# Performance work log

Hardware: AMD Instinct MI355X
Metric: run time of the kernel (lower is better)

The kernel has to match this reference:

```python
import jax, jax.numpy as jnp
import numpy as np

FEATURE_SIZE = 1000000  # padding index == FEATURE_SIZE
NEG_INF = -1e9


def _attn_pool(emb_table, hist_idx, ad_idx):
    # hist_idx: [B, L] int, ad_idx: [B] int
    hist = emb_table[hist_idx]          # [B, L, K] gather
    ad = emb_table[ad_idx]              # [B, K]
    score = jnp.einsum('blk,bk->bl', hist, ad)          # [B, L]
    score = jnp.where(hist_idx != FEATURE_SIZE, score, NEG_INF)
    w = jax.nn.softmax(score, axis=1)
    return jnp.einsum('blk,bl->bk', hist, w)            # [B, K]


def setup_inputs() -> dict:
    key = jax.random.key(0)
    ks = jax.random.split(key, 12)
    B, F, K = 4096, 8, 64
    V = FEATURE_SIZE + 1
    d_in = 3 * K + F * K  # 704
    inp = {
        'feature_idx': jax.random.randint(ks[0], (B, F), 0, FEATURE_SIZE),
        'hist_item': jax.random.randint(ks[1], (B, 350), 0, V),
        'hist_author': jax.random.randint(ks[2], (B, 250), 0, V),
        'hist_music': jax.random.randint(ks[3], (B, 100), 0, V),
        'emb_table': jax.random.normal(ks[4], (V, K), jnp.float32),
        'W1': jax.random.normal(ks[5], (d_in, 512), jnp.float32) * 0.02,
        'b1': jnp.zeros((512,), jnp.float32),
        'W2': jax.random.normal(ks[6], (512, 256), jnp.float32) * 0.02,
        'b2': jnp.zeros((256,), jnp.float32),
        'W3': jax.random.normal(ks[7], (256, 128), jnp.float32) * 0.02,
        'b3': jnp.zeros((128,), jnp.float32),
        'Wo': jax.random.normal(ks[8], (128, 1), jnp.float32) * 0.02,
        'bo': jnp.zeros((1,), jnp.float32),
    }
    return inp


def reference(feature_idx, hist_item, hist_author, hist_music, emb_table,
              W1, b1, W2, b2, W3, b3, Wo, bo):
    # ad indices for the three behavior features: columns 2, 3, 6
    pools = [
        _attn_pool(emb_table, hist_item, feature_idx[:, 2]),
        _attn_pool(emb_table, hist_author, feature_idx[:, 3]),
        _attn_pool(emb_table, hist_music, feature_idx[:, 6]),
    ]
    user_beha = jnp.concatenate(pools, axis=1)                    # [B, 3K]
    B = feature_idx.shape[0]
    ad_emb = emb_table[feature_idx].reshape(B, -1)                # [B, F*K]
    x = jnp.concatenate([user_beha, ad_emb], axis=1)              # [B, 704]
    x = jax.nn.relu(x @ W1 + b1)
    x = jax.nn.relu(x @ W2 + b2)
    x = jax.nn.relu(x @ W3 + b3)
    logits = x @ Wo + bo                                          # [B, 1]
    return logits
```

## Files before the change

kernel.cpp:

```cpp
#include <hip/hip_runtime.h>
#include <cstddef>

#define BATCH   4096
#define PAD_IDX 1000000
#define NEG_INF_F (-1e9f)

typedef __attribute__((ext_vector_type(8))) short bf16x8;
typedef __attribute__((ext_vector_type(4))) float f32x4;
typedef unsigned short u16;

__device__ __forceinline__ u16 f2bf(float f) {
    unsigned u = __float_as_uint(f);
    return (u16)((u + 0x7fffu + ((u >> 16) & 1u)) >> 16);
}
__device__ __forceinline__ float bf2f(u16 b) {
    return __uint_as_float(((unsigned)b) << 16);
}

#define UPD(mm, dd, aa, s, v)                          \
    {                                                  \
        float nm = fmaxf(mm, (s));                     \
        float sc = __expf(mm - nm);                    \
        float e  = __expf((s) - nm);                   \
        dd = fmaf(dd, sc, e);                          \
        aa.x = fmaf(aa.x, sc, e * (v).x);              \
        aa.y = fmaf(aa.y, sc, e * (v).y);              \
        aa.z = fmaf(aa.z, sc, e * (v).z);              \
        aa.w = fmaf(aa.w, sc, e * (v).w);              \
        mm = nm;                                       \
    }

#define MERGE(P)                                                  \
    {                                                             \
        float mo  = __shfl_xor(m, P);                             \
        float d_o = __shfl_xor(d, P);                             \
        float ax = __shfl_xor(acc.x, P);                          \
        float ay = __shfl_xor(acc.y, P);                          \
        float az = __shfl_xor(acc.z, P);                          \
        float aw = __shfl_xor(acc.w, P);                          \
        float nm = fmaxf(m, mo);                                  \
        float sA = __expf(m - nm), sB = __expf(mo - nm);          \
        d = d * sA + d_o * sB;                                    \
        acc.x = acc.x * sA + ax * sB;                             \
        acc.y = acc.y * sA + ay * sB;                             \
        acc.z = acc.z * sA + az * sB;                             \
        acc.w = acc.w * sA + aw * sB;                             \
        m = nm;                                                   \
    }

#define QRED(s)                       \
    s += __shfl_xor(s, 1);            \
    s += __shfl_xor(s, 2);            \
    s += __shfl_xor(s, 4);            \
    s += __shfl_xor(s, 8);

#define DOT4(v, a) ((v).x * (a).x + (v).y * (a).y + (v).z * (a).z + (v).w * (a).w)

__global__ void __launch_bounds__(256) prep_kernel(
    const int* __restrict__ fidx,
    const int* __restrict__ hist_item,
    const int* __restrict__ hist_author,
    const int* __restrict__ hist_music,
    const float* __restrict__ emb,
    const float* __restrict__ W1, const float* __restrict__ W2, const float* __restrict__ W3,
    u16* __restrict__ x,
    u16* __restrict__ w1t, u16* __restrict__ w2t, u16* __restrict__ w3t)
{
    __shared__ float tile[32][33];
    const int blk = blockIdx.x;

    if (blk < 5120) {
        const int w    = blk * 4 + (threadIdx.x >> 6);
        const int lane = threadIdx.x & 63;
        const int t16  = lane & 15;
        const int q    = lane >> 4;

        if (w < 3 * BATCH) {
            const int h = w >> 12;
            const int b = w & (BATCH - 1);
            int L, col, off;
            const int* hrow;
            if (h == 0)      { L = 350; col = 2; off = 0;   hrow = hist_item   + (size_t)b * 350; }
            else if (h == 1) { L = 250; col = 3; off = 64;  hrow = hist_author + (size_t)b * 250; }
            else             { L = 100; col = 6; off = 128; hrow = hist_music  + (size_t)b * 100; }

            const int ad_idx = fidx[b * 8 + col];
            const float4 ad4 = *(const float4*)(emb + (size_t)ad_idx * 64 + 4 * t16);

            float m = NEG_INF_F, d = 0.f;
            float4 acc = make_float4(0.f, 0.f, 0.f, 0.f);
            float mB = NEG_INF_F, dB = 0.f;
            float4 aB = make_float4(0.f, 0.f, 0.f, 0.f);

            int l = 0;
            if (L >= 16) {
                int n0 = hrow[q], n1 = hrow[4 + q], n2 = hrow[8 + q], n3 = hrow[12 + q];
                while (true) {
                    const int i0 = n0, i1 = n1, i2 = n2, i3 = n3;
                    const float4 v0 = *(const float4*)(emb + (size_t)i0 * 64 + 4 * t16);
                    const float4 v1 = *(const float4*)(emb + (size_t)i1 * 64 + 4 * t16);
                    const float4 v2 = *(const float4*)(emb + (size_t)i2 * 64 + 4 * t16);
                    const float4 v3 = *(const float4*)(emb + (size_t)i3 * 64 + 4 * t16);
                    l += 16;
                    const bool more = (l + 16 <= L);
                    if (more) {
                        n0 = hrow[l + q];      n1 = hrow[l + 4 + q];
                        n2 = hrow[l + 8 + q];  n3 = hrow[l + 12 + q];
                    }
                    float s0 = DOT4(v0, ad4);
                    float s1 = DOT4(v1, ad4);
                    float s2 = DOT4(v2, ad4);
                    float s3 = DOT4(v3, ad4);
                    QRED(s0) QRED(s1) QRED(s2) QRED(s3)
                    if (i0 == PAD_IDX) s0 = NEG_INF_F;
                    if (i1 == PAD_IDX) s1 = NEG_INF_F;
                    if (i2 == PAD_IDX) s2 = NEG_INF_F;
                    if (i3 == PAD_IDX) s3 = NEG_INF_F;
                    UPD(m, d, acc, s0, v0)
                    UPD(mB, dB, aB, s1, v1)
                    UPD(m, d, acc, s2, v2)
                    UPD(mB, dB, aB, s3, v3)
                    if (!more) break;
                }
            }
            for (; l < L; l += 4) {
                const int li = l + q;
                const int i0 = (li < L) ? hrow[li] : PAD_IDX;
                const float4 v0 = *(const float4*)(emb + (size_t)i0 * 64 + 4 * t16);
                float s0 = DOT4(v0, ad4);
                QRED(s0)
                if (i0 == PAD_IDX) s0 = NEG_INF_F;
                UPD(m, d, acc, s0, v0)
            }

            {
                float nm = fmaxf(m, mB);
                float eA = __expf(m - nm), eB = __expf(mB - nm);
                d = d * eA + dB * eB;
                acc.x = acc.x * eA + aB.x * eB;
                acc.y = acc.y * eA + aB.y * eB;
                acc.z = acc.z * eA + aB.z * eB;
                acc.w = acc.w * eA + aB.w * eB;
                m = nm;
            }
            MERGE(16)
            MERGE(32)

            if (lane < 16) {
                const float inv = 1.f / d;
                uint2 p;
                p.x = (unsigned)f2bf(acc.x * inv) | ((unsigned)f2bf(acc.y * inv) << 16);
                p.y = (unsigned)f2bf(acc.z * inv) | ((unsigned)f2bf(acc.w * inv) << 16);
                *(uint2*)(x + (size_t)b * 704 + off + 4 * t16) = p;
            }
        } else {
            const int tt = w - 3 * BATCH;
            const int b  = tt >> 1;
            const int f  = ((tt & 1) << 2) + q;
            const int idx = fidx[b * 8 + f];
            const float4 v = *(const float4*)(emb + (size_t)idx * 64 + 4 * t16);
            uint2 p;
            p.x = (unsigned)f2bf(v.x) | ((unsigned)f2bf(v.y) << 16);
            p.y = (unsigned)f2bf(v.z) | ((unsigned)f2bf(v.w) << 16);
            *(uint2*)(x + (size_t)b * 704 + 192 + (size_t)f * 64 + 4 * t16) = p;
        }
    } else {
        int t = blk - 5120;
        const float* W; u16* WT; int K, N, tk, tn;
        if (t < 352)      { W = W1; WT = w1t; K = 704; N = 512; tk = t % 22; tn = t / 22; }
        else if (t < 480) { t -= 352; W = W2; WT = w2t; K = 512; N = 256; tk = t % 16; tn = t / 16; }
        else              { t -= 480; W = W3; WT = w3t; K = 256; N = 128; tk = t % 8;  tn = t / 8;  }
        const int k0 = tk * 32, n0 = tn * 32;
        const int tx = threadIdx.x & 31, ty = threadIdx.x >> 5;
#pragma unroll
        for (int j = 0; j < 4; ++j)
            tile[ty + 8 * j][tx] = W[(size_t)(k0 + ty + 8 * j) * N + n0 + tx];
        __syncthreads();
#pragma unroll
        for (int j = 0; j < 4; ++j)
            WT[(size_t)(n0 + ty + 8 * j) * K + k0 + tx] = f2bf(tile[tx][ty + 8 * j]);
    }
}

template <int BN>
__global__ void __launch_bounds__(256) gemm_mfma(
    const u16* __restrict__ A, const u16* __restrict__ BT,
    const float* __restrict__ bias, u16* __restrict__ C,
    int M, int N, int K)
{
    constexpr int NB = BN / 16;
    __shared__ u16 As[64][40];
    __shared__ u16 Bs[BN][40];

    const int tid  = threadIdx.x;
    const int wave = tid >> 6, lane = tid & 63;
    const int quad = lane >> 4, l16 = lane & 15;
    const int bm = blockIdx.y * 64, bn = blockIdx.x * BN;

    const int srow = tid >> 2;
    const int sk   = (tid & 3) * 8;

    f32x4 acc[NB];
#pragma unroll
    for (int i = 0; i < NB; ++i) acc[i] = (f32x4){0.f, 0.f, 0.f, 0.f};

    const size_t a_base = (size_t)(bm + srow) * K + sk;

    for (int k0 = 0; k0 < K; k0 += 32) {
        *(float4*)&As[srow][sk] = *(const float4*)(A + a_base + k0);
#pragma unroll
        for (int r0 = 0; r0 < BN; r0 += 64) {
            *(float4*)&Bs[r0 + srow][sk] =
                *(const float4*)(BT + (size_t)(bn + r0 + srow) * K + k0 + sk);
        }
        __syncthreads();

        const bf16x8 af = *(const bf16x8*)&As[wave * 16 + l16][quad * 8];
#pragma unroll
        for (int ni = 0; ni < NB; ++ni) {
            const bf16x8 bf = *(const bf16x8*)&Bs[ni * 16 + l16][quad * 8];
            acc[ni] = __builtin_amdgcn_mfma_f32_16x16x32_bf16(af, bf, acc[ni], 0, 0, 0);
        }
        __syncthreads();
    }

#pragma unroll
    for (int ni = 0; ni < NB; ++ni) {
        const int col = bn + ni * 16 + l16;
        const float bv = bias[col];
#pragma unroll
        for (int r = 0; r < 4; ++r) {
            const int row = bm + wave * 16 + quad * 4 + r;
            float v = fmaxf(acc[ni][r] + bv, 0.f);
            C[(size_t)row * N + col] = f2bf(v);
        }
    }
}

__global__ void __launch_bounds__(256) gemm3_out(
    const u16* __restrict__ A, const u16* __restrict__ BT,
    const float* __restrict__ bias,
    const float* __restrict__ Wo, const float* __restrict__ bo,
    float* __restrict__ out)
{
    constexpr int K = 256, NB = 8;
    __shared__ u16 As[64][40];
    __shared__ u16 Bs[128][40];

    const int tid  = threadIdx.x;
    const int wave = tid >> 6, lane = tid & 63;
    const int quad = lane >> 4, l16 = lane & 15;
    const int bm = blockIdx.x * 64;

    const int srow = tid >> 2;
    const int sk   = (tid & 3) * 8;

    f32x4 acc[NB];
#pragma unroll
    for (int i = 0; i < NB; ++i) acc[i] = (f32x4){0.f, 0.f, 0.f, 0.f};

    const size_t a_base = (size_t)(bm + srow) * K + sk;

    for (int k0 = 0; k0 < K; k0 += 32) {
        *(float4*)&As[srow][sk] = *(const float4*)(A + a_base + k0);
#pragma unroll
        for (int r0 = 0; r0 < 128; r0 += 64) {
            *(float4*)&Bs[r0 + srow][sk] =
                *(const float4*)(BT + (size_t)(r0 + srow) * K + k0 + sk);
        }
        __syncthreads();

        const bf16x8 af = *(const bf16x8*)&As[wave * 16 + l16][quad * 8];
#pragma unroll
        for (int ni = 0; ni < NB; ++ni) {
            const bf16x8 bf = *(const bf16x8*)&Bs[ni * 16 + l16][quad * 8];
            acc[ni] = __builtin_amdgcn_mfma_f32_16x16x32_bf16(af, bf, acc[ni], 0, 0, 0);
        }
        __syncthreads();
    }

    float part[4] = {0.f, 0.f, 0.f, 0.f};
#pragma unroll
    for (int ni = 0; ni < NB; ++ni) {
        const int col = ni * 16 + l16;
        const float bv = bias[col];
        const float wv = Wo[col];
#pragma unroll
        for (int r = 0; r < 4; ++r)
            part[r] = fmaf(fmaxf(acc[ni][r] + bv, 0.f), wv, part[r]);
    }
#pragma unroll
    for (int r = 0; r < 4; ++r) {
        part[r] += __shfl_xor(part[r], 1);
        part[r] += __shfl_xor(part[r], 2);
        part[r] += __shfl_xor(part[r], 4);
        part[r] += __shfl_xor(part[r], 8);
    }
    if (l16 == 0) {
        const float b0 = bo[0];
#pragma unroll
        for (int r = 0; r < 4; ++r)
            out[bm + wave * 16 + quad * 4 + r] = part[r] + b0;
    }
}

extern "C" void kernel_launch(void* const* d_in, const int* in_sizes, int n_in,
                              void* d_out, int out_size, void* d_ws, size_t ws_size,
                              hipStream_t stream) {
    const int*   fidx  = (const int*)d_in[0];
    const int*   hitem = (const int*)d_in[1];
    const int*   hauth = (const int*)d_in[2];
    const int*   hmus  = (const int*)d_in[3];
    const float* emb   = (const float*)d_in[4];
    const float* W1 = (const float*)d_in[5];
    const float* b1 = (const float*)d_in[6];
    const float* W2 = (const float*)d_in[7];
    const float* b2 = (const float*)d_in[8];
    const float* W3 = (const float*)d_in[9];
    const float* b3 = (const float*)d_in[10];
    const float* Wo = (const float*)d_in[11];
    const float* bo = (const float*)d_in[12];
    float* out = (float*)d_out;

    u16* x   = (u16*)d_ws;
    u16* h1  = x   + (size_t)BATCH * 704;
    u16* h2  = h1  + (size_t)BATCH * 512;
    u16* w1t = h2  + (size_t)BATCH * 256;
    u16* w2t = w1t + (size_t)704 * 512;
    u16* w3t = w2t + (size_t)512 * 256;

    prep_kernel<<<5632, 256, 0, stream>>>(fidx, hitem, hauth, hmus, emb,
                                          W1, W2, W3, x, w1t, w2t, w3t);

    gemm_mfma<64><<<dim3(512 / 64, BATCH / 64), 256, 0, stream>>>(
        x, w1t, b1, h1, BATCH, 512, 704);
    gemm_mfma<64><<<dim3(256 / 64, BATCH / 64), 256, 0, stream>>>(
        h1, w2t, b2, h2, BATCH, 256, 512);
    gemm3_out<<<BATCH / 64, 256, 0, stream>>>(h2, w3t, b3, Wo, bo, out);
}
```

Baseline: 445.3 us.

## Prefetch embedding table into cache and fuse the layer-2/3/output GEMMs

Adds 2048 leading blocks to the prep kernel that stream-read the whole embedding table, so that the random row gathers of the attention pooling are more likely to hit the large last-level cache. A dummy conditional store keeps the compiler from removing these reads. Separately, the second and third MLP layers and the output projection are merged into one tail kernel over 16-row tiles that keeps h2 in shared memory, which removes a launch and the h2 round trip through global memory. The cost is an extra full-table read of about 256 MB, and each tail block re-reading all of W2T/W3T with smaller tiles.

```diff
diff --git a/kernel.cpp b/kernel.cpp
--- a/kernel.cpp
+++ b/kernel.cpp
@@ -4,6 +4,7 @@
 #define BATCH   4096
 #define PAD_IDX 1000000
 #define NEG_INF_F (-1e9f)
+#define EMB_FLOATS 64000064
 
 typedef __attribute__((ext_vector_type(8))) short bf16x8;
 typedef __attribute__((ext_vector_type(4))) float f32x4;
@@ -12,9 +13,6 @@
 __device__ __forceinline__ u16 f2bf(float f) {
     unsigned u = __float_as_uint(f);
     return (u16)((u + 0x7fffu + ((u >> 16) & 1u)) >> 16);
-}
-__device__ __forceinline__ float bf2f(u16 b) {
-    return __uint_as_float(((unsigned)b) << 16);
 }
 
 #define UPD(mm, dd, aa, s, v)                          \
@@ -68,10 +66,26 @@
 {
     __shared__ float tile[32][33];
     const int blk = blockIdx.x;
-
-    if (blk < 5120) {
-        const int w    = blk * 4 + (threadIdx.x >> 6);
-        const int lane = threadIdx.x & 63;
+    const int tid = threadIdx.x;
+
+    if (blk < 2048) {
+        float s = 0.f;
+        const size_t base = (size_t)blk * 32768 + tid * 4;
+#pragma unroll 8
+        for (int i = 0; i < 32; ++i) {
+            const size_t fi = base + (size_t)i * 1024;
+            if (fi + 4 <= EMB_FLOATS) {
+                const float4 v = *(const float4*)(emb + fi);
+                s += v.x + v.y + v.z + v.w;
+            }
+        }
+        if (s == 1.2345e37f) x[0] = 1;
+        return;
+    }
+
+    if (blk < 7168) {
+        const int w    = (blk - 2048) * 4 + (tid >> 6);
+        const int lane = tid & 63;
         const int t16  = lane & 15;
         const int q    = lane >> 4;
 
@@ -164,22 +178,23 @@
             p.y = (unsigned)f2bf(v.z) | ((unsigned)f2bf(v.w) << 16);
             *(uint2*)(x + (size_t)b * 704 + 192 + (size_t)f * 64 + 4 * t16) = p;
         }
-    } else {
-        int t = blk - 5120;
-        const float* W; u16* WT; int K, N, tk, tn;
-        if (t < 352)      { W = W1; WT = w1t; K = 704; N = 512; tk = t % 22; tn = t / 22; }
-        else if (t < 480) { t -= 352; W = W2; WT = w2t; K = 512; N = 256; tk = t % 16; tn = t / 16; }
-        else              { t -= 480; W = W3; WT = w3t; K = 256; N = 128; tk = t % 8;  tn = t / 8;  }
-        const int k0 = tk * 32, n0 = tn * 32;
-        const int tx = threadIdx.x & 31, ty = threadIdx.x >> 5;
-#pragma unroll
-        for (int j = 0; j < 4; ++j)
-            tile[ty + 8 * j][tx] = W[(size_t)(k0 + ty + 8 * j) * N + n0 + tx];
-        __syncthreads();
-#pragma unroll
-        for (int j = 0; j < 4; ++j)
-            WT[(size_t)(n0 + ty + 8 * j) * K + k0 + tx] = f2bf(tile[tx][ty + 8 * j]);
-    }
+        return;
+    }
+
+    int t = blk - 7168;
+    const float* W; u16* WT; int K, N, tk, tn;
+    if (t < 352)      { W = W1; WT = w1t; K = 704; N = 512; tk = t % 22; tn = t / 22; }
+    else if (t < 480) { t -= 352; W = W2; WT = w2t; K = 512; N = 256; tk = t % 16; tn = t / 16; }
+    else              { t -= 480; W = W3; WT = w3t; K = 256; N = 128; tk = t % 8;  tn = t / 8;  }
+    const int k0 = tk * 32, n0 = tn * 32;
+    const int tx = tid & 31, ty = tid >> 5;
+#pragma unroll
+    for (int j = 0; j < 4; ++j)
+        tile[ty + 8 * j][tx] = W[(size_t)(k0 + ty + 8 * j) * N + n0 + tx];
+    __syncthreads();
+#pragma unroll
+    for (int j = 0; j < 4; ++j)
+        WT[(size_t)(n0 + ty + 8 * j) * K + k0 + tx] = f2bf(tile[tx][ty + 8 * j]);
 }
 
 template <int BN>
@@ -237,71 +252,99 @@
     }
 }
 
-__global__ void __launch_bounds__(256) gemm3_out(
-    const u16* __restrict__ A, const u16* __restrict__ BT,
-    const float* __restrict__ bias,
+__global__ void __launch_bounds__(256) tail_mlp(
+    const u16* __restrict__ h1, const u16* __restrict__ W2T, const u16* __restrict__ W3T,
+    const float* __restrict__ b2, const float* __restrict__ b3,
     const float* __restrict__ Wo, const float* __restrict__ bo,
     float* __restrict__ out)
 {
-    constexpr int K = 256, NB = 8;
-    __shared__ u16 As[64][40];
-    __shared__ u16 Bs[128][40];
+    __shared__ u16 As16[16][40];
+    __shared__ u16 Bs[256][40];
+    __shared__ u16 h2s[16][264];
+    __shared__ float psum[16][4];
 
     const int tid  = threadIdx.x;
     const int wave = tid >> 6, lane = tid & 63;
     const int quad = lane >> 4, l16 = lane & 15;
-    const int bm = blockIdx.x * 64;
-
-    const int srow = tid >> 2;
-    const int sk   = (tid & 3) * 8;
-
-    f32x4 acc[NB];
-#pragma unroll
-    for (int i = 0; i < NB; ++i) acc[i] = (f32x4){0.f, 0.f, 0.f, 0.f};
-
-    const size_t a_base = (size_t)(bm + srow) * K + sk;
-
-    for (int k0 = 0; k0 < K; k0 += 32) {
-        *(float4*)&As[srow][sk] = *(const float4*)(A + a_base + k0);
-#pragma unroll
-        for (int r0 = 0; r0 < 128; r0 += 64) {
-            *(float4*)&Bs[r0 + srow][sk] =
-                *(const float4*)(BT + (size_t)(r0 + srow) * K + k0 + sk);
-        }
-        __syncthreads();
-
-        const bf16x8 af = *(const bf16x8*)&As[wave * 16 + l16][quad * 8];
-#pragma unroll
-        for (int ni = 0; ni < NB; ++ni) {
-            const bf16x8 bf = *(const bf16x8*)&Bs[ni * 16 + l16][quad * 8];
-            acc[ni] = __builtin_amdgcn_mfma_f32_16x16x32_bf16(af, bf, acc[ni], 0, 0, 0);
+    const int r0 = blockIdx.x * 16;
+
+    f32x4 acc2[4];
+#pragma unroll
+    for (int i = 0; i < 4; ++i) acc2[i] = (f32x4){0.f, 0.f, 0.f, 0.f};
+
+    for (int k0 = 0; k0 < 512; k0 += 32) {
+        if (tid < 64)
+            *(float4*)&As16[tid >> 2][(tid & 3) * 8] =
+                *(const float4*)(h1 + (size_t)(r0 + (tid >> 2)) * 512 + k0 + (tid & 3) * 8);
+        {
+            const u16* src = W2T + (size_t)tid * 512 + k0;
+#pragma unroll
+            for (int c = 0; c < 4; ++c)
+                *(float4*)&Bs[tid][c * 8] = *(const float4*)(src + c * 8);
+        }
+        __syncthreads();
+
+        const bf16x8 af = *(const bf16x8*)&As16[l16][quad * 8];
+#pragma unroll
+        for (int ni = 0; ni < 4; ++ni) {
+            const bf16x8 bf = *(const bf16x8*)&Bs[wave * 64 + ni * 16 + l16][quad * 8];
+            acc2[ni] = __builtin_amdgcn_mfma_f32_16x16x32_bf16(af, bf, acc2[ni], 0, 0, 0);
+        }
+        __syncthreads();
+    }
+
+#pragma unroll
+    for (int ni = 0; ni < 4; ++ni) {
+        const int col = wave * 64 + ni * 16 + l16;
+        const float bv = b2[col];
+#pragma unroll
+        for (int r = 0; r < 4; ++r)
+            h2s[quad * 4 + r][col] = f2bf(fmaxf(acc2[ni][r] + bv, 0.f));
+    }
+    __syncthreads();
+
+    f32x4 acc3[2];
+#pragma unroll
+    for (int i = 0; i < 2; ++i) acc3[i] = (f32x4){0.f, 0.f, 0.f, 0.f};
+
+    for (int k0 = 0; k0 < 256; k0 += 32) {
+        if (tid < 128) {
+            const u16* src = W3T + (size_t)tid * 256 + k0;
+#pragma unroll
+            for (int c = 0; c < 4; ++c)
+                *(float4*)&Bs[tid][c * 8] = *(const float4*)(src + c * 8);
+        }
+        __syncthreads();
+
+        const bf16x8 af = *(const bf16x8*)&h2s[l16][k0 + quad * 8];
+#pragma unroll
+        for (int ni = 0; ni < 2; ++ni) {
+            const bf16x8 bf = *(const bf16x8*)&Bs[wave * 32 + ni * 16 + l16][quad * 8];
+            acc3[ni] = __builtin_amdgcn_mfma_f32_16x16x32_bf16(af, bf, acc3[ni], 0, 0, 0);
         }
         __syncthreads();
     }
 
     float part[4] = {0.f, 0.f, 0.f, 0.f};
 #pragma unroll
-    for (int ni = 0; ni < NB; ++ni) {
-        const int col = ni * 16 + l16;
-        const float bv = bias[col];
+    for (int ni = 0; ni < 2; ++ni) {
+        const int col = wave * 32 + ni * 16 + l16;
+        const float bv = b3[col];
         const float wv = Wo[col];
 #pragma unroll
         for (int r = 0; r < 4; ++r)
-            part[r] = fmaf(fmaxf(acc[ni][r] + bv, 0.f), wv, part[r]);
-    }
-#pragma unroll
-    for (int r = 0; r < 4; ++r) {
-        part[r] += __shfl_xor(part[r], 1);
-        part[r] += __shfl_xor(part[r], 2);
-        part[r] += __shfl_xor(part[r], 4);
-        part[r] += __shfl_xor(part[r], 8);
-    }
+            part[r] = fmaf(fmaxf(acc3[ni][r] + bv, 0.f), wv, part[r]);
+    }
+#pragma unroll
+    for (int r = 0; r < 4; ++r) { QRED(part[r]) }
     if (l16 == 0) {
-        const float b0 = bo[0];
 #pragma unroll
         for (int r = 0; r < 4; ++r)
-            out[bm + wave * 16 + quad * 4 + r] = part[r] + b0;
-    }
+            psum[quad * 4 + r][wave] = part[r];
+    }
+    __syncthreads();
+    if (tid < 16)
+        out[r0 + tid] = psum[tid][0] + psum[tid][1] + psum[tid][2] + psum[tid][3] + bo[0];
 }
 
 extern "C" void kernel_launch(void* const* d_in, const int* in_sizes, int n_in,
@@ -324,17 +367,15 @@
 
     u16* x   = (u16*)d_ws;
     u16* h1  = x   + (size_t)BATCH * 704;
-    u16* h2  = h1  + (size_t)BATCH * 512;
-    u16* w1t = h2  + (size_t)BATCH * 256;
+    u16* w1t = h1  + (size_t)BATCH * 512;
     u16* w2t = w1t + (size_t)704 * 512;
     u16* w3t = w2t + (size_t)512 * 256;
 
-    prep_kernel<<<5632, 256, 0, stream>>>(fidx, hitem, hauth, hmus, emb,
+    prep_kernel<<<7680, 256, 0, stream>>>(fidx, hitem, hauth, hmus, emb,
                                           W1, W2, W3, x, w1t, w2t, w3t);
 
     gemm_mfma<64><<<dim3(512 / 64, BATCH / 64), 256, 0, stream>>>(
         x, w1t, b1, h1, BATCH, 512, 704);
-    gemm_mfma<64><<<dim3(256 / 64, BATCH / 64), 256, 0, stream>>>(
-        h1, w2t, b2, h2, BATCH, 256, 512);
-    gemm3_out<<<BATCH / 64, 256, 0, stream>>>(h2, w3t, b3, Wo, bo, out);
-}
+
+    tail_mlp<<<BATCH / 16, 256, 0, stream>>>(h1, w2t, w3t, b2, b3, Wo, bo, out);
+}
```

Measured after the change: 503.8 us. 1.13x slower.
